# Kernel optimization log

Hardware: AMD Instinct MI355X
Metric: run time of the kernel (lower is better)

Reference implementation:

```python
import jax, jax.numpy as jnp
import numpy as np

INPUT_SIZE = 968
HIDDEN = 128
ESP = 1e-6


def _gru_scan(xp, w_hh, b_hh):
    # xp: [T, B, 3H] precomputed input projections; returns [T, B, H]
    B = xp.shape[1]
    h0 = jnp.zeros((B, HIDDEN), dtype=xp.dtype)

    def step(h, xp_t):
        gi_r, gi_z, gi_n = jnp.split(xp_t, 3, axis=-1)
        gh = h @ w_hh.T + b_hh
        gh_r, gh_z, gh_n = jnp.split(gh, 3, axis=-1)
        r = jax.nn.sigmoid(gi_r + gh_r)
        z = jax.nn.sigmoid(gi_z + gh_z)
        n = jnp.tanh(gi_n + r * gh_n)
        h_new = (1.0 - z) * n + z * h
        return h_new, h_new

    _, hs = jax.lax.scan(step, h0, xp)
    return hs


def _bigru_ln(x, w_ih_f, w_hh_f, b_ih_f, b_hh_f,
              w_ih_b, w_hh_b, b_ih_b, b_hh_b, ln_w, ln_b):
    # x: [B, T, D] (batch_first)
    # precompute input projections as one big GEMM per direction
    xp_f = jnp.einsum('btd,gd->btg', x, w_ih_f) + b_ih_f  # [B,T,3H]
    xp_b = jnp.einsum('btd,gd->btg', x, w_ih_b) + b_ih_b
    xp_f = jnp.swapaxes(xp_f, 0, 1)  # [T,B,3H]
    xp_b = jnp.swapaxes(xp_b, 0, 1)[::-1]  # reversed time for backward dir

    h_f = _gru_scan(xp_f, w_hh_f, b_hh_f)          # [T,B,H]
    h_b = _gru_scan(xp_b, w_hh_b, b_hh_b)[::-1]    # [T,B,H], un-reverse

    out = jnp.concatenate([h_f, h_b], axis=-1)     # [T,B,2H]
    out = jnp.swapaxes(out, 0, 1)                  # [B,T,2H]

    # LayerNormal: uses unbiased std (torch.std default, ddof=1), clamped
    mu = jnp.mean(out, axis=-1, keepdims=True)
    sigma = jnp.std(out, axis=-1, keepdims=True, ddof=1)
    sigma = jnp.maximum(sigma, ESP)
    return (out - mu) / sigma * ln_w + ln_b


def setup_inputs() -> dict:
    key = jax.random.key(0)
    ks = jax.random.split(key, 10)
    B, T = 64, 512
    s_ih = 1.0 / np.sqrt(HIDDEN)
    u = lambda k, shape: jax.random.uniform(k, shape, jnp.float32, -s_ih, s_ih)
    return {
        'x': jax.random.normal(ks[0], (B, T, INPUT_SIZE), jnp.float32),
        'w_ih_f': u(ks[1], (3 * HIDDEN, INPUT_SIZE)),
        'w_hh_f': u(ks[2], (3 * HIDDEN, HIDDEN)),
        'b_ih_f': u(ks[3], (3 * HIDDEN,)),
        'b_hh_f': u(ks[4], (3 * HIDDEN,)),
        'w_ih_b': u(ks[5], (3 * HIDDEN, INPUT_SIZE)),
        'w_hh_b': u(ks[6], (3 * HIDDEN, HIDDEN)),
        'b_ih_b': u(ks[7], (3 * HIDDEN,)),
        'b_hh_b': u(ks[8], (3 * HIDDEN,)),
        'ln_w': jnp.ones((2 * HIDDEN,), jnp.float32),
        'ln_b': jnp.zeros((2 * HIDDEN,), jnp.float32),
    }


def reference(x, w_ih_f, w_hh_f, b_ih_f, b_hh_f,
              w_ih_b, w_hh_b, b_ih_b, b_hh_b, ln_w, ln_b):
    return _bigru_ln(x, w_ih_f, w_hh_f, b_ih_f, b_hh_f,
                     w_ih_b, w_hh_b, b_ih_b, b_hh_b, ln_w, ln_b)
```

## Files before the change

kernel.cpp:

```cpp
#include <hip/hip_runtime.h>
#include <stdint.h>


#define LOG2E 1.4426950408889634f
#define TT 512
#define D_IN 968
#define KP 992
#define NOUT 768
#define HID 128

typedef __attribute__((ext_vector_type(8))) short short8;
typedef __attribute__((ext_vector_type(4))) float f32x4;
typedef __attribute__((ext_vector_type(4))) unsigned int u32x4;
typedef __attribute__((ext_vector_type(2))) unsigned int u32x2;

__device__ __forceinline__ unsigned short f2bf(float f) {
  unsigned u = __builtin_bit_cast(unsigned, f);
  u += 0x7FFFu + ((u >> 16) & 1u);
  return (unsigned short)(u >> 16);
}
__device__ __forceinline__ unsigned pack2bf(float a, float b) {
  return (unsigned)f2bf(a) | ((unsigned)f2bf(b) << 16);
}
__device__ __forceinline__ float exp2_(float x) { return __builtin_amdgcn_exp2f(x); }
__device__ __forceinline__ float rcp_(float x)  { return __builtin_amdgcn_rcpf(x); }

__device__ __forceinline__ void async_load16(const void* g, void* l) {
  __builtin_amdgcn_global_load_lds(
      (const __attribute__((address_space(1))) unsigned int*)g,
      (__attribute__((address_space(3))) unsigned int*)l, 16, 0, 0);
}

__device__ __forceinline__ void wg_barrier_lds() {
  asm volatile("s_waitcnt lgkmcnt(0)\n\ts_barrier" ::: "memory");
}

#define WIH_BYTES (NOUT * KP * 2)
#define WHH_BYTES (NOUT * HID * 2)
#define BIAS_BYTES 3072
#define BASE_OFF (WIH_BYTES + WHH_BYTES + BIAS_BYTES)
#define XBF_BYTES ((size_t)32768 * KP * 2)
#define XP_BYTES ((size_t)32768 * NOUT * 4)

__global__ __launch_bounds__(256) void kx_convert(const float* __restrict__ X,
                                                  unsigned short* __restrict__ Xb) {
  const long row = blockIdx.x;
  const int t = threadIdx.x;
  if (t < 242) {
    f32x4 v = *(const f32x4*)(X + row * D_IN + t * 4);
    u32x2 p = {pack2bf(v.x, v.y), pack2bf(v.z, v.w)};
    *(u32x2*)(Xb + row * KP + t * 4) = p;
  } else if (t < 248) {
    *(u32x2*)(Xb + row * KP + t * 4) = (u32x2){0, 0};
  }
}

__global__ __launch_bounds__(256) void k0_convert(
    const float* __restrict__ wihf, const float* __restrict__ whhf,
    const float* __restrict__ bihf, const float* __restrict__ wihb,
    const float* __restrict__ whhb, const float* __restrict__ bihb,
    const float* __restrict__ bhhf, const float* __restrict__ bhhb,
    unsigned short* __restrict__ wih16, unsigned short* __restrict__ whh16,
    float* __restrict__ bias_s) {
  int blk = blockIdx.x, tid = threadIdx.x;
  if (blk < NOUT) {
    int n = blk;
    float sc = ((n % 384) < 256) ? LOG2E : 2.0f * LOG2E;
    const float* src = (n < 384) ? (wihf + (long)n * D_IN) : (wihb + (long)(n - 384) * D_IN);
    for (int c = 0; c < 4; c++) {
      int k = c * 256 + tid;
      if (k < KP) {
        float v = (k < D_IN) ? src[k] * sc : 0.0f;
        wih16[(long)n * KP + k] = f2bf(v);
      }
    }
  } else if (blk < NOUT + 96) {
    int e0 = ((blk - NOUT) * 256 + tid) * 4;
    for (int i = 0; i < 4; i++) {
      int e = e0 + i;
      int m = e >> 7, k = e & 127;
      float sc = ((m % 384) < 256) ? LOG2E : 2.0f * LOG2E;
      float v = (m < 384) ? whhf[m * HID + k] : whhb[(m - 384) * HID + k];
      whh16[e] = f2bf(v * sc);
    }
  } else {
    for (int c = 0; c < 3; c++) {
      int n = c * 256 + tid;
      if (n < NOUT) {
        int g = (n % 384) >> 7;
        float sc = (g < 2) ? LOG2E : 2.0f * LOG2E;
        float bi = (n < 384) ? bihf[n] : bihb[n - 384];
        float bh = (n < 384) ? bhhf[n] : bhhb[n - 384];
        float v = (g < 2) ? (bi + bh) : bi;
        bias_s[n] = v * sc;
      }
    }
  }
}

__global__ __launch_bounds__(256, 2) void k1_gemm_fast(
    const unsigned short* __restrict__ Xb, const unsigned short* __restrict__ W,
    const float* __restrict__ bias_s, float* __restrict__ XP) {
  __shared__ unsigned short As[128 * 32];
  __shared__ unsigned short Bs[128 * 32];

  const int tid = threadIdx.x;
  const int lane = tid & 63, w = tid >> 6;
  const int q = lane >> 4, l15 = lane & 15;
  const int wr = w >> 1, wc = w & 1;
  const int nt = blockIdx.x;
  const int mt = blockIdx.y;
  const long R0 = (long)mt * 128;
  const int C0 = nt * 128;

  f32x4 acc[4][4];
#pragma unroll
  for (int i = 0; i < 4; i++)
#pragma unroll
    for (int j = 0; j < 4; j++) acc[i][j] = {0.f, 0.f, 0.f, 0.f};

  for (int it = 0; it < 31; it++) {
    const int k0 = it * 32;
#pragma unroll
    for (int c = 0; c < 2; c++) {
      int idx = c * 256 + w * 64 + lane;
      int row = idx >> 2, koff = (idx & 3) * 8;
      async_load16(Xb + (R0 + row) * KP + k0 + koff,
                   ((char*)As) + (c * 256 + w * 64) * 16);
      async_load16(W + (long)(C0 + row) * KP + k0 + koff,
                   ((char*)Bs) + (c * 256 + w * 64) * 16);
    }
    __syncthreads();
    short8 af[4], bf[4];
#pragma unroll
    for (int i = 0; i < 4; i++)
      af[i] = *(const short8*)&As[(wr * 64 + i * 16 + l15) * 32 + q * 8];
#pragma unroll
    for (int j = 0; j < 4; j++)
      bf[j] = *(const short8*)&Bs[(wc * 64 + j * 16 + l15) * 32 + q * 8];
#pragma unroll
    for (int i = 0; i < 4; i++)
#pragma unroll
      for (int j = 0; j < 4; j++)
        acc[i][j] = __builtin_amdgcn_mfma_f32_16x16x32_bf16(af[i], bf[j], acc[i][j], 0, 0, 0);
    __syncthreads();
  }
  float bv[4];
#pragma unroll
  for (int j = 0; j < 4; j++) bv[j] = bias_s[C0 + wc * 64 + j * 16 + l15];
#pragma unroll
  for (int i = 0; i < 4; i++)
#pragma unroll
    for (int j = 0; j < 4; j++) {
      int col = C0 + wc * 64 + j * 16 + l15;
      long Rb = R0 + wr * 64 + i * 16 + q * 4;
#pragma unroll
      for (int r = 0; r < 4; r++)
        XP[(Rb + r) * NOUT + col] = acc[i][j][r] + bv[j];
    }
}

#define AS_STRIDE 40
__global__ __launch_bounds__(256, 2) void k1_gemm_slow(
    const float* __restrict__ X, const unsigned short* __restrict__ W,
    const float* __restrict__ bias_s, float* __restrict__ XP) {
  __shared__ unsigned short As[128 * AS_STRIDE];
  __shared__ unsigned short Bs[128 * 32];
  const int tid = threadIdx.x;
  const int lane = tid & 63, w = tid >> 6;
  const int q = lane >> 4, l15 = lane & 15;
  const int wr = w >> 1, wc = w & 1;
  const int nt = blockIdx.x, mt = blockIdx.y;
  const long R0 = (long)mt * 128;
  const int C0 = nt * 128;
  const int ar = tid >> 1, ahf = tid & 1;
  f32x4 acc[4][4];
#pragma unroll
  for (int i = 0; i < 4; i++)
#pragma unroll
    for (int j = 0; j < 4; j++) acc[i][j] = {0.f, 0.f, 0.f, 0.f};
  const float* arow = X + (R0 + ar) * D_IN;
  for (int it = 0; it < 31; it++) {
    int k0 = it * 32;
    unsigned pk[8];
#pragma unroll
    for (int c = 0; c < 4; c++) {
      int kc = k0 + ahf * 16 + c * 4;
      kc = (kc <= 964) ? kc : 964;
      f32x4 v = *(const f32x4*)(arow + kc);
      pk[c * 2 + 0] = pack2bf(v.x, v.y);
      pk[c * 2 + 1] = pack2bf(v.z, v.w);
    }
    unsigned short* adst = &As[ar * AS_STRIDE + ahf * 16];
    *(u32x4*)adst = (u32x4){pk[0], pk[1], pk[2], pk[3]};
    *(u32x4*)(adst + 8) = (u32x4){pk[4], pk[5], pk[6], pk[7]};
#pragma unroll
    for (int c = 0; c < 2; c++) {
      int idx = c * 256 + w * 64 + lane;
      int brow = idx >> 2, koff = (idx & 3) * 8;
      async_load16(W + (long)(C0 + brow) * KP + k0 + koff,
                   ((char*)Bs) + (c * 256 + w * 64) * 16);
    }
    __syncthreads();
    short8 af[4], bf[4];
#pragma unroll
    for (int i = 0; i < 4; i++)
      af[i] = *(const short8*)&As[(wr * 64 + i * 16 + l15) * AS_STRIDE + q * 8];
#pragma unroll
    for (int j = 0; j < 4; j++)
      bf[j] = *(const short8*)&Bs[(wc * 64 + j * 16 + l15) * 32 + q * 8];
#pragma unroll
    for (int i = 0; i < 4; i++)
#pragma unroll
      for (int j = 0; j < 4; j++)
        acc[i][j] = __builtin_amdgcn_mfma_f32_16x16x32_bf16(af[i], bf[j], acc[i][j], 0, 0, 0);
    __syncthreads();
  }
  float bv[4];
#pragma unroll
  for (int j = 0; j < 4; j++) bv[j] = bias_s[C0 + wc * 64 + j * 16 + l15];
#pragma unroll
  for (int i = 0; i < 4; i++)
#pragma unroll
    for (int j = 0; j < 4; j++) {
      int col = C0 + wc * 64 + j * 16 + l15;
      long Rb = R0 + wr * 64 + i * 16 + q * 4;
#pragma unroll
      for (int r = 0; r < 4; r++)
        XP[(Rb + r) * NOUT + col] = acc[i][j][r] + bv[j];
    }
}

__device__ __forceinline__ f32x4 gru_gate(f32x4 accR, f32x4 accZ, f32x4 accN,
                                          f32x4 gr, f32x4 gz, f32x4 gn,
                                          f32x4 bh2, f32x4 h) {
  f32x4 pr = gr + accR;
  f32x4 pz = gz + accZ;
  f32x4 er, ez;
#pragma unroll
  for (int i = 0; i < 4; i++) er[i] = exp2_(-pr[i]);
#pragma unroll
  for (int i = 0; i < 4; i++) ez[i] = exp2_(-pz[i]);
  f32x4 dr = er + 1.0f, dz = ez + 1.0f;
  f32x4 r, z;
#pragma unroll
  for (int i = 0; i < 4; i++) r[i] = rcp_(dr[i]);
#pragma unroll
  for (int i = 0; i < 4; i++) z[i] = rcp_(dz[i]);
  f32x4 pn = gn + r * (accN + bh2);
  f32x4 en;
#pragma unroll
  for (int i = 0; i < 4; i++) en[i] = exp2_(pn[i]);
  f32x4 dn = en + 1.0f, invn;
#pragma unroll
  for (int i = 0; i < 4; i++) invn[i] = rcp_(dn[i]);
  f32x4 n = 1.0f - 2.0f * invn;
  return n + z * (h - n);
}

#define PF 4
#define MFMA_BF16 __builtin_amdgcn_mfma_f32_16x16x32_bf16

#define K2_STEP(U, REFILL)                                                    \
  {                                                                           \
    const unsigned short* hb = ((U) & 1) ? hrd1 : hrd0;                       \
    short8 b0 = *(const short8*)(hb + ch0);                                   \
    short8 b1 = *(const short8*)(hb + ch1);                                   \
    short8 b2 = *(const short8*)(hb + ch2);                                   \
    short8 b3 = *(const short8*)(hb + ch3);                                   \
    f32x4 cgR = gRr[U], cgZ = gZr[U], cgN = gNr[U];                           \
    if (REFILL) {                                                             \
      gRr[U] = *(const f32x4*)(gp);                                           \
      gZr[U] = *(const f32x4*)(gp + 128);                                     \
      gNr[U] = *(const f32x4*)(gp + 256);                                     \
      gp += gstep;                                                            \
    }                                                                         \
    const f32x4 zz = {0.f, 0.f, 0.f, 0.f};                                    \
    f32x4 aR0 = MFMA_BF16(afr[0][0], b0, zz, 0, 0, 0);                        \
    f32x4 aZ0 = MFMA_BF16(afr[1][0], b0, zz, 0, 0, 0);                        \
    f32x4 aN0 = MFMA_BF16(afr[2][0], b0, zz, 0, 0, 0);                        \
    f32x4 aR1 = MFMA_BF16(afr[0][2], b2, zz, 0, 0, 0);                        \
    f32x4 aZ1 = MFMA_BF16(afr[1][2], b2, zz, 0, 0, 0);                        \
    f32x4 aN1 = MFMA_BF16(afr[2][2], b2, zz, 0, 0, 0);                        \
    aR0 = MFMA_BF16(afr[0][1], b1, aR0, 0, 0, 0);                             \
    aZ0 = MFMA_BF16(afr[1][1], b1, aZ0, 0, 0, 0);                             \
    aN0 = MFMA_BF16(afr[2][1], b1, aN0, 0, 0, 0);                             \
    aR1 = MFMA_BF16(afr[0][3], b3, aR1, 0, 0, 0);                             \
    aZ1 = MFMA_BF16(afr[1][3], b3, aZ1, 0, 0, 0);                             \
    aN1 = MFMA_BF16(afr[2][3], b3, aN1, 0, 0, 0);                             \
    f32x4 hnew = gru_gate(aR0 + aR1, aZ0 + aZ1, aN0 + aN1,                    \
                          cgR, cgZ, cgN, bh2, h);                             \
    h = hnew;                                                                 \
    u32x2 hv = {pack2bf(hnew[0], hnew[1]), pack2bf(hnew[2], hnew[3])};        \
    *(u32x2*)(((U) & 1) ? hwr0 : hwr1) = hv;                                  \
    *(f32x4*)op = hnew;                                                       \
    op += ostep;                                                              \
    wg_barrier_lds();                                                         \
  }

__global__ __launch_bounds__(512) void k2_gru(
    const unsigned short* __restrict__ WHH, const float* __restrict__ XP,
    const float* __restrict__ bhh_f, const float* __restrict__ bhh_b,
    float* __restrict__ OUT) {
  __shared__ unsigned short Hl[2][16 * 128];

  const int tid = threadIdx.x;
  const int lane = tid & 63, w = tid >> 6;
  const int q = lane >> 4, b = lane & 15;
  const int dir = blockIdx.x & 1, bg = blockIdx.x >> 1;
  const int j0 = w * 16 + q * 4;

  for (int i = tid; i < 2 * 16 * 128; i += 512) ((unsigned short*)Hl)[i] = 0;

  short8 afr[3][4];
#pragma unroll
  for (int g = 0; g < 3; g++)
#pragma unroll
    for (int kt = 0; kt < 4; kt++) {
      int row = dir * 384 + g * 128 + w * 16 + b;
      afr[g][kt] = *(const short8*)(WHH + (long)row * HID + kt * 32 + q * 8);
    }
  const float* bhh = dir ? bhh_b : bhh_f;
  f32x4 bh2 = (*(const f32x4*)(bhh + 256 + j0)) * (2.0f * LOG2E);

  const long gstep = dir ? -(long)NOUT : (long)NOUT;
  const long ostep = dir ? -256L : 256L;
  const int td0 = dir ? (TT - 1) : 0;
  const float* gp = XP + ((long)(bg * 16 + b) * TT + td0) * NOUT + dir * 384 + j0;
  float* op = OUT + ((long)(bg * 16 + b) * TT + td0) * 256 + dir * 128 + j0;

  f32x4 gRr[PF], gZr[PF], gNr[PF];
#pragma unroll
  for (int u = 0; u < PF; u++) {
    gRr[u] = *(const f32x4*)(gp);
    gZr[u] = *(const f32x4*)(gp + 128);
    gNr[u] = *(const f32x4*)(gp + 256);
    gp += gstep;
  }

  const int ch0 = ((0 * 4 + q) ^ (b & 7)) * 8;
  const int ch1 = ((1 * 4 + q) ^ (b & 7)) * 8;
  const int ch2 = ((2 * 4 + q) ^ (b & 7)) * 8;
  const int ch3 = ((3 * 4 + q) ^ (b & 7)) * 8;
  const int chw = (((j0 >> 3) ^ (b & 7)) * 8) + (j0 & 7);
  const unsigned short* hrd0 = &Hl[0][b * 128];
  const unsigned short* hrd1 = &Hl[1][b * 128];
  unsigned short* hwr0 = &Hl[0][b * 128 + chw];
  unsigned short* hwr1 = &Hl[1][b * 128 + chw];

  f32x4 h = {0.f, 0.f, 0.f, 0.f};
  __syncthreads();

  for (int t0 = 0; t0 < TT - PF; t0 += PF) {
    K2_STEP(0, 1)
    K2_STEP(1, 1)
    K2_STEP(2, 1)
    K2_STEP(3, 1)
  }
  K2_STEP(0, 0)
  K2_STEP(1, 0)
  K2_STEP(2, 0)
  K2_STEP(3, 0)
}

__global__ __launch_bounds__(256) void k3_ln(float* __restrict__ OUT,
                                             const float* __restrict__ lnw,
                                             const float* __restrict__ lnb) {
  const int tid = threadIdx.x, lane = tid & 63, w = tid >> 6;
  const long row = (long)blockIdx.x * 4 + w;
  float* p = OUT + row * 256 + lane * 4;
  f32x4 x = *(const f32x4*)p;
  float s = x[0] + x[1] + x[2] + x[3];
  float s2 = x[0] * x[0] + x[1] * x[1] + x[2] * x[2] + x[3] * x[3];
#pragma unroll
  for (int m = 1; m < 64; m <<= 1) {
    s += __shfl_xor(s, m, 64);
    s2 += __shfl_xor(s2, m, 64);
  }
  float mu = s * (1.0f / 256.0f);
  float var = (s2 - s * mu) * (1.0f / 255.0f);
  var = fmaxf(var, 0.0f);
  float sig = fmaxf(sqrtf(var), 1e-6f);
  float inv = 1.0f / sig;
  f32x4 wv = *(const f32x4*)(lnw + lane * 4);
  f32x4 bv = *(const f32x4*)(lnb + lane * 4);
  f32x4 y;
#pragma unroll
  for (int i = 0; i < 4; i++) y[i] = (x[i] - mu) * inv * wv[i] + bv[i];
  *(f32x4*)p = y;
}

extern "C" void kernel_launch(void* const* d_in, const int* in_sizes, int n_in,
                              void* d_out, int out_size, void* d_ws, size_t ws_size,
                              hipStream_t stream) {
  const float* x = (const float*)d_in[0];
  const float* wihf = (const float*)d_in[1];
  const float* whhf = (const float*)d_in[2];
  const float* bihf = (const float*)d_in[3];
  const float* bhhf = (const float*)d_in[4];
  const float* wihb = (const float*)d_in[5];
  const float* whhb = (const float*)d_in[6];
  const float* bihb = (const float*)d_in[7];
  const float* bhhb = (const float*)d_in[8];
  const float* lnw = (const float*)d_in[9];
  const float* lnb = (const float*)d_in[10];

  char* ws = (char*)d_ws;
  unsigned short* wih16 = (unsigned short*)ws;
  unsigned short* whh16 = (unsigned short*)(ws + WIH_BYTES);
  float* bias_s = (float*)(ws + WIH_BYTES + WHH_BYTES);
  float* out = (float*)d_out;

  const size_t need_fast = (size_t)BASE_OFF + XBF_BYTES + XP_BYTES;

  hipLaunchKernelGGL(k0_convert, dim3(768 + 96 + 1), dim3(256), 0, stream,
                     wihf, whhf, bihf, wihb, whhb, bihb, bhhf, bhhb,
                     wih16, whh16, bias_s);

  float* xp;
  if (ws_size >= need_fast) {
    unsigned short* xbf = (unsigned short*)(ws + BASE_OFF);
    xp = (float*)(ws + BASE_OFF + XBF_BYTES);
    hipLaunchKernelGGL(kx_convert, dim3(32768), dim3(256), 0, stream, x, xbf);
    hipLaunchKernelGGL(k1_gemm_fast, dim3(6, 256), dim3(256), 0, stream,
                       xbf, wih16, bias_s, xp);
  } else {
    xp = (float*)(ws + BASE_OFF);
    hipLaunchKernelGGL(k1_gemm_slow, dim3(6, 256), dim3(256), 0, stream,
                       x, wih16, bias_s, xp);
  }
  hipLaunchKernelGGL(k2_gru, dim3(8), dim3(512), 0, stream, whh16, xp, bhhf, bhhb, out);
  hipLaunchKernelGGL(k3_ln, dim3(8192), dim3(256), 0, stream, out, lnw, lnb);
}
```

Baseline: 703.3 us.

## Halve GRU recurrence workgroup to four waves, each computing two hidden-unit tiles

The recurrent GRU kernel now runs 256 threads per block instead of 512. Each wave owns 32 hidden units (two 16-row MFMA tiles per gate) and keeps twice as many W_hh fragments in registers. The per-step workgroup barrier then synchronises fewer waves, and each wave has more independent MFMA chains to hide latency on the serial time loop. In exchange, register pressure roughly doubles and the input-projection prefetch depth drops from 4 to 2 timesteps, which may expose global-load latency.

New measurement: 728.4 us. 1.04x slower.

```diff
diff --git a/kernel.cpp b/kernel.cpp
--- a/kernel.cpp
+++ b/kernel.cpp
@@ -258,47 +258,70 @@
   return n + z * (h - n);
 }
 
-#define PF 4
+#define PF 2
 #define MFMA_BF16 __builtin_amdgcn_mfma_f32_16x16x32_bf16
 
 #define K2_STEP(U, REFILL)                                                    \
   {                                                                           \
     const unsigned short* hb = ((U) & 1) ? hrd1 : hrd0;                       \
-    short8 b0 = *(const short8*)(hb + ch0);                                   \
-    short8 b1 = *(const short8*)(hb + ch1);                                   \
-    short8 b2 = *(const short8*)(hb + ch2);                                   \
-    short8 b3 = *(const short8*)(hb + ch3);                                   \
-    f32x4 cgR = gRr[U], cgZ = gZr[U], cgN = gNr[U];                           \
+    short8 f0 = *(const short8*)(hb + ch0);                                   \
+    short8 f1 = *(const short8*)(hb + ch1);                                   \
+    short8 f2 = *(const short8*)(hb + ch2);                                   \
+    short8 f3 = *(const short8*)(hb + ch3);                                   \
+    f32x4 cR0 = gg[0][0][U], cZ0 = gg[0][1][U], cN0 = gg[0][2][U];            \
+    f32x4 cR1 = gg[1][0][U], cZ1 = gg[1][1][U], cN1 = gg[1][2][U];            \
     if (REFILL) {                                                             \
-      gRr[U] = *(const f32x4*)(gp);                                           \
-      gZr[U] = *(const f32x4*)(gp + 128);                                     \
-      gNr[U] = *(const f32x4*)(gp + 256);                                     \
+      gg[0][0][U] = *(const f32x4*)(gp);                                      \
+      gg[0][1][U] = *(const f32x4*)(gp + 128);                                \
+      gg[0][2][U] = *(const f32x4*)(gp + 256);                                \
+      gg[1][0][U] = *(const f32x4*)(gp + 16);                                 \
+      gg[1][1][U] = *(const f32x4*)(gp + 144);                                \
+      gg[1][2][U] = *(const f32x4*)(gp + 272);                                \
       gp += gstep;                                                            \
     }                                                                         \
     const f32x4 zz = {0.f, 0.f, 0.f, 0.f};                                    \
-    f32x4 aR0 = MFMA_BF16(afr[0][0], b0, zz, 0, 0, 0);                        \
-    f32x4 aZ0 = MFMA_BF16(afr[1][0], b0, zz, 0, 0, 0);                        \
-    f32x4 aN0 = MFMA_BF16(afr[2][0], b0, zz, 0, 0, 0);                        \
-    f32x4 aR1 = MFMA_BF16(afr[0][2], b2, zz, 0, 0, 0);                        \
-    f32x4 aZ1 = MFMA_BF16(afr[1][2], b2, zz, 0, 0, 0);                        \
-    f32x4 aN1 = MFMA_BF16(afr[2][2], b2, zz, 0, 0, 0);                        \
-    aR0 = MFMA_BF16(afr[0][1], b1, aR0, 0, 0, 0);                             \
-    aZ0 = MFMA_BF16(afr[1][1], b1, aZ0, 0, 0, 0);                             \
-    aN0 = MFMA_BF16(afr[2][1], b1, aN0, 0, 0, 0);                             \
-    aR1 = MFMA_BF16(afr[0][3], b3, aR1, 0, 0, 0);                             \
-    aZ1 = MFMA_BF16(afr[1][3], b3, aZ1, 0, 0, 0);                             \
-    aN1 = MFMA_BF16(afr[2][3], b3, aN1, 0, 0, 0);                             \
-    f32x4 hnew = gru_gate(aR0 + aR1, aZ0 + aZ1, aN0 + aN1,                    \
-                          cgR, cgZ, cgN, bh2, h);                             \
-    h = hnew;                                                                 \
-    u32x2 hv = {pack2bf(hnew[0], hnew[1]), pack2bf(hnew[2], hnew[3])};        \
-    *(u32x2*)(((U) & 1) ? hwr0 : hwr1) = hv;                                  \
-    *(f32x4*)op = hnew;                                                       \
+                             \
+    f32x4 aR0 = MFMA_BF16(afr[0][0][0], f0, zz, 0, 0, 0);                     \
+    f32x4 aZ0 = MFMA_BF16(afr[0][1][0], f0, zz, 0, 0, 0);                     \
+    f32x4 aN0 = MFMA_BF16(afr[0][2][0], f0, zz, 0, 0, 0);                     \
+    aR0 = MFMA_BF16(afr[0][0][1], f1, aR0, 0, 0, 0);                          \
+    aZ0 = MFMA_BF16(afr[0][1][1], f1, aZ0, 0, 0, 0);                          \
+    aN0 = MFMA_BF16(afr[0][2][1], f1, aN0, 0, 0, 0);                          \
+    aR0 = MFMA_BF16(afr[0][0][2], f2, aR0, 0, 0, 0);                          \
+    aZ0 = MFMA_BF16(afr[0][1][2], f2, aZ0, 0, 0, 0);                          \
+    aN0 = MFMA_BF16(afr[0][2][2], f2, aN0, 0, 0, 0);                          \
+    aR0 = MFMA_BF16(afr[0][0][3], f3, aR0, 0, 0, 0);                          \
+    aZ0 = MFMA_BF16(afr[0][1][3], f3, aZ0, 0, 0, 0);                          \
+    aN0 = MFMA_BF16(afr[0][2][3], f3, aN0, 0, 0, 0);                          \
+                                           \
+    f32x4 aR1 = MFMA_BF16(afr[1][0][0], f0, zz, 0, 0, 0);                     \
+    f32x4 aZ1 = MFMA_BF16(afr[1][1][0], f0, zz, 0, 0, 0);                     \
+    f32x4 aN1 = MFMA_BF16(afr[1][2][0], f0, zz, 0, 0, 0);                     \
+    aR1 = MFMA_BF16(afr[1][0][1], f1, aR1, 0, 0, 0);                          \
+    aZ1 = MFMA_BF16(afr[1][1][1], f1, aZ1, 0, 0, 0);                          \
+    aN1 = MFMA_BF16(afr[1][2][1], f1, aN1, 0, 0, 0);                          \
+    aR1 = MFMA_BF16(afr[1][0][2], f2, aR1, 0, 0, 0);                          \
+    aZ1 = MFMA_BF16(afr[1][1][2], f2, aZ1, 0, 0, 0);                          \
+    aN1 = MFMA_BF16(afr[1][2][2], f2, aN1, 0, 0, 0);                          \
+    aR1 = MFMA_BF16(afr[1][0][3], f3, aR1, 0, 0, 0);                          \
+    aZ1 = MFMA_BF16(afr[1][1][3], f3, aZ1, 0, 0, 0);                          \
+    aN1 = MFMA_BF16(afr[1][2][3], f3, aN1, 0, 0, 0);                          \
+                                         \
+    f32x4 hn0 = gru_gate(aR0, aZ0, aN0, cR0, cZ0, cN0, bh20, h0);             \
+    h0 = hn0;                                                                 \
+    u32x2 hv0 = {pack2bf(hn0[0], hn0[1]), pack2bf(hn0[2], hn0[3])};           \
+    *(u32x2*)(((U) & 1) ? hw0_b0 : hw0_b1) = hv0;                             \
+    *(f32x4*)op = hn0;                                                        \
+    f32x4 hn1 = gru_gate(aR1, aZ1, aN1, cR1, cZ1, cN1, bh21, h1);             \
+    h1 = hn1;                                                                 \
+    u32x2 hv1 = {pack2bf(hn1[0], hn1[1]), pack2bf(hn1[2], hn1[3])};           \
+    *(u32x2*)(((U) & 1) ? hw1_b0 : hw1_b1) = hv1;                             \
+    *(f32x4*)(op + 16) = hn1;                                                 \
     op += ostep;                                                              \
     wg_barrier_lds();                                                         \
   }
 
-__global__ __launch_bounds__(512) void k2_gru(
+__global__ __launch_bounds__(256, 1) void k2_gru(
     const unsigned short* __restrict__ WHH, const float* __restrict__ XP,
     const float* __restrict__ bhh_f, const float* __restrict__ bhh_b,
     float* __restrict__ OUT) {
@@ -308,20 +331,23 @@
   const int lane = tid & 63, w = tid >> 6;
   const int q = lane >> 4, b = lane & 15;
   const int dir = blockIdx.x & 1, bg = blockIdx.x >> 1;
-  const int j0 = w * 16 + q * 4;
-
-  for (int i = tid; i < 2 * 16 * 128; i += 512) ((unsigned short*)Hl)[i] = 0;
-
-  short8 afr[3][4];
-#pragma unroll
-  for (int g = 0; g < 3; g++)
-#pragma unroll
-    for (int kt = 0; kt < 4; kt++) {
-      int row = dir * 384 + g * 128 + w * 16 + b;
-      afr[g][kt] = *(const short8*)(WHH + (long)row * HID + kt * 32 + q * 8);
-    }
+  const int j0 = w * 32 + q * 4;
+
+  for (int i = tid; i < 2 * 16 * 128; i += 256) ((unsigned short*)Hl)[i] = 0;
+
+  short8 afr[2][3][4];
+#pragma unroll
+  for (int c = 0; c < 2; c++)
+#pragma unroll
+    for (int g = 0; g < 3; g++)
+#pragma unroll
+      for (int kt = 0; kt < 4; kt++) {
+        int row = dir * 384 + g * 128 + w * 32 + c * 16 + b;
+        afr[c][g][kt] = *(const short8*)(WHH + (long)row * HID + kt * 32 + q * 8);
+      }
   const float* bhh = dir ? bhh_b : bhh_f;
-  f32x4 bh2 = (*(const f32x4*)(bhh + 256 + j0)) * (2.0f * LOG2E);
+  f32x4 bh20 = (*(const f32x4*)(bhh + 256 + j0)) * (2.0f * LOG2E);
+  f32x4 bh21 = (*(const f32x4*)(bhh + 256 + j0 + 16)) * (2.0f * LOG2E);
 
   const long gstep = dir ? -(long)NOUT : (long)NOUT;
   const long ostep = dir ? -256L : 256L;
@@ -329,12 +355,15 @@
   const float* gp = XP + ((long)(bg * 16 + b) * TT + td0) * NOUT + dir * 384 + j0;
   float* op = OUT + ((long)(bg * 16 + b) * TT + td0) * 256 + dir * 128 + j0;
 
-  f32x4 gRr[PF], gZr[PF], gNr[PF];
+  f32x4 gg[2][3][PF];
 #pragma unroll
   for (int u = 0; u < PF; u++) {
-    gRr[u] = *(const f32x4*)(gp);
-    gZr[u] = *(const f32x4*)(gp + 128);
-    gNr[u] = *(const f32x4*)(gp + 256);
+    gg[0][0][u] = *(const f32x4*)(gp);
+    gg[0][1][u] = *(const f32x4*)(gp + 128);
+    gg[0][2][u] = *(const f32x4*)(gp + 256);
+    gg[1][0][u] = *(const f32x4*)(gp + 16);
+    gg[1][1][u] = *(const f32x4*)(gp + 144);
+    gg[1][2][u] = *(const f32x4*)(gp + 272);
     gp += gstep;
   }
 
@@ -342,25 +371,25 @@
   const int ch1 = ((1 * 4 + q) ^ (b & 7)) * 8;
   const int ch2 = ((2 * 4 + q) ^ (b & 7)) * 8;
   const int ch3 = ((3 * 4 + q) ^ (b & 7)) * 8;
-  const int chw = (((j0 >> 3) ^ (b & 7)) * 8) + (j0 & 7);
+  const int cw0 = (((4 * w + 0 + (q >> 1)) ^ (b & 7)) * 8) + (q & 1) * 4;
+  const int cw1 = (((4 * w + 2 + (q >> 1)) ^ (b & 7)) * 8) + (q & 1) * 4;
   const unsigned short* hrd0 = &Hl[0][b * 128];
   const unsigned short* hrd1 = &Hl[1][b * 128];
-  unsigned short* hwr0 = &Hl[0][b * 128 + chw];
-  unsigned short* hwr1 = &Hl[1][b * 128 + chw];
-
-  f32x4 h = {0.f, 0.f, 0.f, 0.f};
+  unsigned short* hw0_b0 = &Hl[0][b * 128 + cw0];
+  unsigned short* hw0_b1 = &Hl[1][b * 128 + cw0];
+  unsigned short* hw1_b0 = &Hl[0][b * 128 + cw1];
+  unsigned short* hw1_b1 = &Hl[1][b * 128 + cw1];
+
+  f32x4 h0 = {0.f, 0.f, 0.f, 0.f};
+  f32x4 h1 = {0.f, 0.f, 0.f, 0.f};
   __syncthreads();
 
   for (int t0 = 0; t0 < TT - PF; t0 += PF) {
     K2_STEP(0, 1)
     K2_STEP(1, 1)
-    K2_STEP(2, 1)
-    K2_STEP(3, 1)
   }
   K2_STEP(0, 0)
   K2_STEP(1, 0)
-  K2_STEP(2, 0)
-  K2_STEP(3, 0)
 }
 
 __global__ __launch_bounds__(256) void k3_ln(float* __restrict__ OUT,
@@ -429,6 +458,6 @@
     hipLaunchKernelGGL(k1_gemm_slow, dim3(6, 256), dim3(256), 0, stream,
                        x, wih16, bias_s, xp);
   }
-  hipLaunchKernelGGL(k2_gru, dim3(8), dim3(512), 0, stream, whh16, xp, bhhf, bhhb, out);
+  hipLaunchKernelGGL(k2_gru, dim3(8), dim3(256), 0, stream, whh16, xp, bhhf, bhhb, out);
   hipLaunchKernelGGL(k3_ln, dim3(8192), dim3(256), 0, stream, out, lnw, lnb);
 }
```
